# Performance work log

Hardware: AMD Instinct MI355X
Metric: run time of the kernel (lower is better)

Reference implementation:

```python
import jax, jax.numpy as jnp
import numpy as np

VOCAB, N_CLASS, H, E = 50000, 6, 512, 300
B, S = 256, 512


def setup_inputs() -> dict:
    key = jax.random.key(0)
    ks = jax.random.split(key, 10)
    return {
        "seq": jax.random.randint(ks[0], (B, S), 0, VOCAB),
        "classes": jnp.arange(N_CLASS),
        "embed_W": jax.random.normal(ks[1], (VOCAB, E), jnp.float32) * 0.1,
        "embed_class_W": jax.random.normal(ks[2], (N_CLASS, H), jnp.float32) * 0.1,
        "W_ih": jax.random.normal(ks[3], (3 * H, E), jnp.float32) * 0.05,
        "W_hh": jax.random.normal(ks[4], (3 * H, H), jnp.float32) * 0.05,
        "b_ih": jax.random.normal(ks[5], (3 * H,), jnp.float32) * 0.05,
        "b_hh": jax.random.normal(ks[6], (3 * H,), jnp.float32) * 0.05,
        "attend": jax.random.normal(ks[7], (H, H), jnp.float32) * 0.1,
        "W_cls": jax.random.normal(ks[8], (2, H), jnp.float32) * 0.05,
        "b_cls": jax.random.normal(ks[9], (2,), jnp.float32) * 0.05,
    }


def _gru_scan(xs, W_ih, W_hh, b_ih, b_hh):
    # xs: [S, B, E]; torch GRUCell semantics
    h0 = jnp.zeros((xs.shape[1], W_hh.shape[1]), xs.dtype)

    def step(h, x):
        gi = x @ W_ih.T + b_ih            # [B, 3H]
        gh = h @ W_hh.T + b_hh            # [B, 3H]
        i_r, i_z, i_n = jnp.split(gi, 3, axis=-1)
        h_r, h_z, h_n = jnp.split(gh, 3, axis=-1)
        r = jax.nn.sigmoid(i_r + h_r)
        z = jax.nn.sigmoid(i_z + h_z)
        n = jnp.tanh(i_n + r * h_n)
        h_new = (1.0 - z) * n + z * h
        return h_new, h_new

    _, hs = jax.lax.scan(step, h0, xs)
    return hs  # [S, B, H]


def reference(seq, classes, embed_W, embed_class_W, W_ih, W_hh, b_ih, b_hh,
              attend, W_cls, b_cls):
    pad_mask = (seq > 0).astype(embed_W.dtype)          # [B, S]
    seq_emb = jnp.tanh(embed_W[seq])                    # [B, S, E]
    hs = _gru_scan(seq_emb.transpose(1, 0, 2), W_ih, W_hh, b_ih, b_hh)
    seq_repr = hs.transpose(1, 0, 2)                    # [B, S, H]

    class_emb = embed_class_W[classes]                  # [C, H]
    attn = jnp.tanh(class_emb) @ attend                 # [C, H]
    # scores[c,b,s] = tanh(attn)[c] . seq_repr[b,s], masked
    scores = jnp.einsum('ch,bsh->cbs', jnp.tanh(attn), seq_repr)
    scores = scores * pad_mask[None, :, :]
    ctx = jnp.einsum('cbs,bsh->cbh', jnp.tanh(scores), seq_repr)  # [C, B, H]
    logits = jnp.tanh(ctx) @ W_cls.T + b_cls            # [C, B, 2]
    return jax.nn.log_softmax(logits, axis=-1)
```

## Files before the change

### kernel.cpp

```cpp
#include <hip/hip_runtime.h>
#include <cstdint>
#include <cstddef>

#define NB 256
#define NS 512
#define NE 300
#define NH 512

using f32x4 = __attribute__((ext_vector_type(4))) float;
using s16x8 = __attribute__((ext_vector_type(8))) short;

static __device__ __forceinline__ unsigned short f2bf(float f) {
  unsigned u = __float_as_uint(f);
  u += 0x7FFFu + ((u >> 16) & 1u);
  return (unsigned short)(u >> 16);
}
static __device__ __forceinline__ float bf2f(unsigned short h) {
  return __uint_as_float(((unsigned)h) << 16);
}
static __device__ __forceinline__ float fast_tanh(float x) {
  float xc = fminf(fmaxf(x, -9.f), 9.f);
  float e = __expf(2.f * xc);
  return (e - 1.f) / (e + 1.f);
}
static __device__ __forceinline__ float sigm(float x) {
  return 1.f / (1.f + __expf(-x));
}

__global__ void k_zero(unsigned short* __restrict__ h_ex, unsigned* __restrict__ flags) {
  int i = blockIdx.x * 256 + threadIdx.x;
  unsigned long long* p = (unsigned long long*)(h_ex + (size_t)i * 16);
  #pragma unroll
  for (int j = 0; j < 4; ++j)
    __hip_atomic_store(p + j, 0ull, __ATOMIC_RELAXED, __HIP_MEMORY_SCOPE_AGENT);
  if (i < 4096)
    __hip_atomic_store(flags + i, 0u, __ATOMIC_RELAXED, __HIP_MEMORY_SCOPE_AGENT);
}

__global__ __launch_bounds__(256) void k_xemb(const int* __restrict__ seq,
                                              const float* __restrict__ embed_W,
                                              unsigned short* __restrict__ x_pre) {
  const long long total = (long long)NB * NS * 40;
  for (long long t = (long long)blockIdx.x * 256 + threadIdx.x; t < total;
       t += (long long)gridDim.x * 256) {
    int c = (int)(t % 40);
    long long p = t / 40;
    int s = (int)(p % NS);
    int b = (int)(p / NS);
    int g_b = b >> 4, r = b & 15;
    float vals[8];
    if (c < 38) {
      int id = seq[(size_t)b * NS + s];
      const float* ep = embed_W + (size_t)id * NE;
      if (c < 37) {
        f32x4 u0 = *(const f32x4*)(ep + c * 8);
        f32x4 u1 = *(const f32x4*)(ep + c * 8 + 4);
        vals[0]=u0[0];vals[1]=u0[1];vals[2]=u0[2];vals[3]=u0[3];
        vals[4]=u1[0];vals[5]=u1[1];vals[6]=u1[2];vals[7]=u1[3];
      } else {
        #pragma unroll
        for (int jj = 0; jj < 8; ++jj) { int cc = 296 + jj; vals[jj] = (cc < NE) ? ep[cc] : 0.f; }
      }
    } else {
      #pragma unroll
      for (int jj = 0; jj < 8; ++jj) vals[jj] = 0.f;
    }
    s16x8 pv;
    #pragma unroll
    for (int jj = 0; jj < 8; ++jj) pv[jj] = (short)f2bf(fast_tanh(vals[jj]));
    *(s16x8*)(x_pre + (((size_t)g_b * NS + s) * 16 + r) * 320 + c * 8) = pv;
  }
}

__global__ __launch_bounds__(256) void k_amat(const int* __restrict__ classes,
                                              const float* __restrict__ ecw,
                                              const float* __restrict__ attend,
                                              unsigned short* __restrict__ a_bf) {
  __shared__ float tc[6][512];
  const int tid = threadIdx.x, j = blockIdx.x;
  for (int i = tid; i < 6 * 512; i += 256) {
    int c = i >> 9, hp = i & 511;
    tc[c][hp] = fast_tanh(ecw[(size_t)classes[c] * 512 + hp]);
  }
  __syncthreads();
  #pragma unroll
  for (int i = 0; i < 4; ++i) {
    int task = tid + 256 * i;
    int c = task >> 6, hl = task & 63;
    int h = j * 64 + hl;
    float v = 0.f;
    if (c < 6) {
      float acc = 0.f;
      for (int hp = 0; hp < 512; ++hp) acc += tc[c][hp] * attend[(size_t)hp * 512 + h];
      v = fast_tanh(acc);
    }
    a_bf[c * 512 + h] = f2bf(v);
  }
}

__global__ __launch_bounds__(384) void k_gru(
    const int* __restrict__ seq, const float* __restrict__ embed_W,
    const float* __restrict__ W_ih, const float* __restrict__ W_hh,
    const float* __restrict__ b_ih, const float* __restrict__ b_hh,
    unsigned short* __restrict__ h_ex, unsigned* __restrict__ flags,
    unsigned short* __restrict__ seq_repr,
    const unsigned short* __restrict__ x_pre, int xpre)
{
  __shared__ unsigned short x_lds[2][16][328];
  __shared__ unsigned short h_lds[16][520];
  __shared__ float rz_lds[2][16][32];

  const int tid = threadIdx.x;
  const int w = tid >> 6, l = tid & 63, lo = l & 15, hi = l >> 4;
  const int bid = blockIdx.x;
  const int g_b = (bid & 7) * 2 + (bid >> 7);
  const int g_c = (bid >> 3) & 15;

  const int gg = w >> 1;
  const int cb = (w & 1) * 16;
  const int jrow = gg * 512 + g_c * 32 + cb + lo;

  s16x8 whh[16];
  #pragma unroll
  for (int kt = 0; kt < 16; ++kt) {
    const float* p = W_hh + (size_t)jrow * 512 + kt * 32 + hi * 8;
    f32x4 a0 = *(const f32x4*)p;
    f32x4 a1 = *(const f32x4*)(p + 4);
    s16x8 v;
    v[0]=(short)f2bf(a0[0]); v[1]=(short)f2bf(a0[1]); v[2]=(short)f2bf(a0[2]); v[3]=(short)f2bf(a0[3]);
    v[4]=(short)f2bf(a1[0]); v[5]=(short)f2bf(a1[1]); v[6]=(short)f2bf(a1[2]); v[7]=(short)f2bf(a1[3]);
    whh[kt] = v;
  }
  s16x8 wih[10];
  #pragma unroll
  for (int kt = 0; kt < 10; ++kt) {
    s16x8 v;
    #pragma unroll
    for (int jj = 0; jj < 8; ++jj) {
      int k = kt * 32 + hi * 8 + jj;
      float f = (k < NE) ? W_ih[(size_t)jrow * NE + k] : 0.f;
      v[jj] = (short)f2bf(f);
    }
    wih[kt] = v;
  }
  const float bsum = b_ih[jrow] + b_hh[jrow];
  const float bni = b_ih[jrow], bnh = b_hh[jrow];

  float hcar[4] = {0.f, 0.f, 0.f, 0.f};
  const unsigned* flg = flags + g_b * 32;

  const int xt = tid - 64;
  const int xr0 = (xt >= 0) ? (xt / 40) : 0,          xc0 = (xt >= 0) ? (xt % 40) : 0;
  const int xr1 = (xt >= 0) ? ((xt + 320) / 40) : 0,  xc1 = (xt >= 0) ? ((xt + 320) % 40) : 0;

  auto do_gather = [&](int ss) {
    const int buf = ss & 1;
    #pragma unroll
    for (int i = 0; i < 2; ++i) {
      int task = tid + 384 * i;
      if (task < 640) {
        int r = task & 15, grp = task >> 4;
        float vals[8];
        if (grp < 38) {
          int id = seq[(size_t)(g_b * 16 + r) * NS + ss];
          const float* ep = embed_W + (size_t)id * NE;
          if (grp < 37) {
            f32x4 u0 = *(const f32x4*)(ep + grp * 8);
            f32x4 u1 = *(const f32x4*)(ep + grp * 8 + 4);
            vals[0]=u0[0];vals[1]=u0[1];vals[2]=u0[2];vals[3]=u0[3];
            vals[4]=u1[0];vals[5]=u1[1];vals[6]=u1[2];vals[7]=u1[3];
          } else {
            #pragma unroll
            for (int jj = 0; jj < 8; ++jj) { int cc = 296 + jj; vals[jj] = (cc < NE) ? ep[cc] : 0.f; }
          }
        } else {
          #pragma unroll
          for (int jj = 0; jj < 8; ++jj) vals[jj] = 0.f;
        }
        s16x8 pv;
        #pragma unroll
        for (int jj = 0; jj < 8; ++jj) pv[jj] = (short)f2bf(fast_tanh(vals[jj]));
        *(s16x8*)&x_lds[buf][r][grp * 8] = pv;
      }
    }
  };

  if (xpre) {
    if (w >= 1) {
      const unsigned short* src = x_pre + ((size_t)g_b * NS + 0) * (16 * 320);
      s16x8 v0 = *(const s16x8*)(src + xr0 * 320 + xc0 * 8);
      s16x8 v1 = *(const s16x8*)(src + xr1 * 320 + xc1 * 8);
      *(s16x8*)&x_lds[0][xr0][xc0 * 8] = v0;
      *(s16x8*)&x_lds[0][xr1][xc1 * 8] = v1;
    }
  } else {
    do_gather(0);
  }
  __syncthreads();

  #pragma unroll 1
  for (int s = 0; s < NS; ++s) {
    const bool xpf = xpre && (s + 1 < NS) && (w >= 1);
    s16x8 xv0, xv1;
    if (xpf) {
      const unsigned short* src = x_pre + ((size_t)g_b * NS + (s + 1)) * (16 * 320);
      xv0 = *(const s16x8*)(src + xr0 * 320 + xc0 * 8);
      xv1 = *(const s16x8*)(src + xr1 * 320 + xc1 * 8);
    } else if (!xpre && s + 1 < NS) {
      do_gather(s + 1);
    }

    f32x4 ax = {0.f,0.f,0.f,0.f};
    #pragma unroll
    for (int kt = 0; kt < 10; ++kt) {
      s16x8 af = *(const s16x8*)&x_lds[s & 1][lo][kt * 32 + hi * 8];
      ax = __builtin_amdgcn_mfma_f32_16x16x32_bf16(af, wih[kt], ax, 0, 0, 0);
    }

    if (s > 0 && tid < 64) {
      const unsigned* fp = flg + (l & 31);
      int guard = 0;
      for (;;) {
        unsigned f = __hip_atomic_load(fp, __ATOMIC_RELAXED, __HIP_MEMORY_SCOPE_AGENT);
        if (__all(f >= (unsigned)s)) break;
        __builtin_amdgcn_s_sleep(1);
        if (++guard > (1 << 22)) break;
      }
    }
    __syncthreads();

    const unsigned short* hsrc = h_ex + ((size_t)(s & 1) * 16 + g_b) * (16 * 512);
    #pragma unroll
    for (int i = 0; i < 6; ++i) {
      int task = tid + 384 * i;
      if (task < 2048) {
        int r = task >> 7, c4 = task & 127;
        unsigned long long v = __hip_atomic_load(
            (const unsigned long long*)(hsrc + r * 512 + c4 * 4),
            __ATOMIC_RELAXED, __HIP_MEMORY_SCOPE_AGENT);
        *(unsigned long long*)&h_lds[r][c4 * 4] = v;
      }
    }
    __syncthreads();

    if (xpf) {
      *(s16x8*)&x_lds[(s + 1) & 1][xr0][xc0 * 8] = xv0;
      *(s16x8*)&x_lds[(s + 1) & 1][xr1][xc1 * 8] = xv1;
    }

    f32x4 ah0 = {0.f,0.f,0.f,0.f}, ah1 = {0.f,0.f,0.f,0.f};
    #pragma unroll
    for (int kt = 0; kt < 16; kt += 2) {
      s16x8 af0 = *(const s16x8*)&h_lds[lo][kt * 32 + hi * 8];
      s16x8 af1 = *(const s16x8*)&h_lds[lo][(kt + 1) * 32 + hi * 8];
      ah0 = __builtin_amdgcn_mfma_f32_16x16x32_bf16(af0, whh[kt], ah0, 0, 0, 0);
      ah1 = __builtin_amdgcn_mfma_f32_16x16x32_bf16(af1, whh[kt + 1], ah1, 0, 0, 0);
    }
    f32x4 ah = ah0 + ah1;

    if (w < 4) {
      #pragma unroll
      for (int j = 0; j < 4; ++j) {
        int row = hi * 4 + j;
        rz_lds[gg][row][cb + lo] = ax[j] + ah[j] + bsum;
      }
    }
    __syncthreads();

    if (w >= 4) {
      unsigned short* hdst = h_ex + ((size_t)((s + 1) & 1) * 16 + g_b) * (16 * 512);
      const int cpr = cb + lo;
      const int col = g_c * 32 + cpr;
      unsigned words[4];
      #pragma unroll
      for (int j = 0; j < 4; ++j) {
        int row = hi * 4 + j;
        float rr = sigm(rz_lds[0][row][cpr]);
        float zz = sigm(rz_lds[1][row][cpr]);
        float nn = fast_tanh(ax[j] + bni + rr * (ah[j] + bnh));
        float hn = (1.f - zz) * nn + zz * hcar[j];
        hcar[j] = hn;
        unsigned myb = (unsigned)f2bf(hn);
        unsigned other = __shfl_xor(myb, 1);
        words[j] = myb | (other << 16);
      }
      if ((lo & 1) == 0) {
        #pragma unroll
        for (int j = 0; j < 4; ++j)
          __hip_atomic_store((unsigned*)(hdst + (hi * 4 + j) * 512 + col), words[j],
                             __ATOMIC_RELAXED, __HIP_MEMORY_SCOPE_AGENT);
      }
      asm volatile("s_waitcnt vmcnt(0)" ::: "memory");
      if (l == 0)
        __hip_atomic_store((unsigned*)(flags + g_b * 32 + g_c * 2 + (w & 1)),
                           (unsigned)(s + 1),
                           __ATOMIC_RELAXED, __HIP_MEMORY_SCOPE_AGENT);
      if ((lo & 1) == 0) {
        #pragma unroll
        for (int j = 0; j < 4; ++j)
          *(unsigned*)(seq_repr + ((size_t)(g_b * 16 + hi * 4 + j) * NS + s) * NH + col) = words[j];
      }
    }
  }
}

__global__ __launch_bounds__(256) void k_attn(const int* __restrict__ seq,
                                              const unsigned short* __restrict__ seq_repr,
                                              const unsigned short* __restrict__ a_bf,
                                              const float* __restrict__ W_cls,
                                              const float* __restrict__ b_cls,
                                              float* __restrict__ out)
{
  __shared__ unsigned short V[32][520];
  __shared__ float P[32][8];
  __shared__ float red[4][12];
  const int tid = threadIdx.x, b = blockIdx.x;
  const int w = tid >> 6, l = tid & 63, lo = l & 15, hi = l >> 4;

  s16x8 afr[16];
  #pragma unroll
  for (int kt = 0; kt < 16; ++kt)
    afr[kt] = *(const s16x8*)(a_bf + (size_t)lo * 512 + kt * 32 + hi * 8);

  float ctx0[6] = {0,0,0,0,0,0}, ctx1[6] = {0,0,0,0,0,0};
  const unsigned short* vbase = seq_repr + (size_t)b * NS * NH;

  for (int sc = 0; sc < 16; ++sc) {
    #pragma unroll 4
    for (int i = 0; i < 8; ++i) {
      int task = tid + 256 * i;
      int sl = task >> 6, grp = task & 63;
      s16x8 v = *(const s16x8*)(vbase + (size_t)(sc * 32 + sl) * NH + grp * 8);
      *(s16x8*)&V[sl][grp * 8] = v;
    }
    __syncthreads();
    if (w < 2) {
      f32x4 acc = {0.f,0.f,0.f,0.f};
      int sl0 = w * 16;
      #pragma unroll
      for (int kt = 0; kt < 16; ++kt) {
        s16x8 af = *(const s16x8*)&V[sl0 + lo][kt * 32 + hi * 8];
        acc = __builtin_amdgcn_mfma_f32_16x16x32_bf16(af, afr[kt], acc, 0, 0, 0);
      }
      if (lo < 8) {
        #pragma unroll
        for (int j = 0; j < 4; ++j) {
          int sl = sl0 + hi * 4 + j;
          float p = 0.f;
          if (lo < 6) {
            int s = sc * 32 + sl;
            p = (seq[(size_t)b * NS + s] > 0) ? fast_tanh(acc[j]) : 0.f;
          }
          P[sl][lo] = p;
        }
      }
    }
    __syncthreads();
    #pragma unroll 2
    for (int sl = 0; sl < 32; ++sl) {
      unsigned v2 = *(const unsigned*)&V[sl][tid * 2];
      float v0 = bf2f((unsigned short)(v2 & 0xFFFFu));
      float v1 = bf2f((unsigned short)(v2 >> 16));
      #pragma unroll
      for (int c = 0; c < 6; ++c) {
        float p = P[sl][c];
        ctx0[c] += p * v0; ctx1[c] += p * v1;
      }
    }
    __syncthreads();
  }

  float pl[12];
  #pragma unroll
  for (int c = 0; c < 6; ++c) {
    float t0 = fast_tanh(ctx0[c]), t1 = fast_tanh(ctx1[c]);
    pl[c * 2 + 0] = t0 * W_cls[tid * 2] + t1 * W_cls[tid * 2 + 1];
    pl[c * 2 + 1] = t0 * W_cls[512 + tid * 2] + t1 * W_cls[512 + tid * 2 + 1];
  }
  #pragma unroll
  for (int i = 0; i < 12; ++i) {
    float v = pl[i];
    for (int off = 32; off > 0; off >>= 1) v += __shfl_down(v, off);
    if (l == 0) red[w][i] = v;
  }
  __syncthreads();
  if (tid < 6) {
    int c = tid;
    float l0 = red[0][c*2] + red[1][c*2] + red[2][c*2] + red[3][c*2] + b_cls[0];
    float l1 = red[0][c*2+1] + red[1][c*2+1] + red[2][c*2+1] + red[3][c*2+1] + b_cls[1];
    float m = fmaxf(l0, l1);
    float lse = m + logf(__expf(l0 - m) + __expf(l1 - m));
    out[c * 512 + b * 2 + 0] = l0 - lse;
    out[c * 512 + b * 2 + 1] = l1 - lse;
  }
}

extern "C" void kernel_launch(void* const* d_in, const int* in_sizes, int n_in,
                              void* d_out, int out_size, void* d_ws, size_t ws_size,
                              hipStream_t stream) {
  const int*   seq      = (const int*)d_in[0];
  const int*   classes  = (const int*)d_in[1];
  const float* embed_W  = (const float*)d_in[2];
  const float* ecw      = (const float*)d_in[3];
  const float* W_ih     = (const float*)d_in[4];
  const float* W_hh     = (const float*)d_in[5];
  const float* b_ih     = (const float*)d_in[6];
  const float* b_hh     = (const float*)d_in[7];
  const float* attend   = (const float*)d_in[8];
  const float* W_cls    = (const float*)d_in[9];
  const float* b_cls    = (const float*)d_in[10];
  float* out = (float*)d_out;

  char* ws = (char*)d_ws;
  const size_t OFF_HEX  = 134217728;
  const size_t OFF_FLG  = OFF_HEX + 524288;
  const size_t OFF_ABF  = OFF_FLG + 16384;
  const size_t OFF_XPRE = OFF_ABF + 16384;
  const size_t XPRE_BYTES = (size_t)16 * NS * 16 * 320 * 2;
  unsigned short* seq_repr = (unsigned short*)ws;
  unsigned short* h_ex     = (unsigned short*)(ws + OFF_HEX);
  unsigned*       flags    = (unsigned*)(ws + OFF_FLG);
  unsigned short* a_bf     = (unsigned short*)(ws + OFF_ABF);
  unsigned short* x_pre    = (unsigned short*)(ws + OFF_XPRE);
  const int xpre = (ws_size >= OFF_XPRE + XPRE_BYTES) ? 1 : 0;

  hipLaunchKernelGGL(k_zero, dim3(64), dim3(256), 0, stream, h_ex, flags);
  hipLaunchKernelGGL(k_amat, dim3(8), dim3(256), 0, stream, classes, ecw, attend, a_bf);
  if (xpre)
    hipLaunchKernelGGL(k_xemb, dim3(2048), dim3(256), 0, stream, seq, embed_W, x_pre);
  hipLaunchKernelGGL(k_gru, dim3(256), dim3(384), 0, stream,
                     seq, embed_W, W_ih, W_hh, b_ih, b_hh, h_ex, flags, seq_repr,
                     x_pre, xpre);
  hipLaunchKernelGGL(k_attn, dim3(256), dim3(256), 0, stream,
                     seq, seq_repr, a_bf, W_cls, b_cls, out);
}
```

Measured before the change: 2.244 ms.

## Replace flag-based step barrier with step-tagged hidden-state words

Each bf16 hidden value is now stored in a 32-bit word with the step number in its upper half. Consumers load the whole hidden tile and re-poll only the words whose tag does not match yet, so the separate flag array, the vmcnt drain and the flag store are gone. This removes a store-then-flag round trip and a pre-read barrier from the recurrent critical path. In exchange, the hidden exchange buffer doubles in size, every thread spins on global memory, and the spin-loop guard is much lower than before.

```diff
diff --git a/kernel.cpp b/kernel.cpp
--- a/kernel.cpp
+++ b/kernel.cpp
@@ -27,14 +27,12 @@
   return 1.f / (1.f + __expf(-x));
 }
 
-__global__ void k_zero(unsigned short* __restrict__ h_ex, unsigned* __restrict__ flags) {
+__global__ void k_zero(unsigned* __restrict__ h_w) {
   int i = blockIdx.x * 256 + threadIdx.x;
-  unsigned long long* p = (unsigned long long*)(h_ex + (size_t)i * 16);
-  #pragma unroll
-  for (int j = 0; j < 4; ++j)
+  unsigned long long* p = (unsigned long long*)(h_w + (size_t)i * 16);
+  #pragma unroll
+  for (int j = 0; j < 8; ++j)
     __hip_atomic_store(p + j, 0ull, __ATOMIC_RELAXED, __HIP_MEMORY_SCOPE_AGENT);
-  if (i < 4096)
-    __hip_atomic_store(flags + i, 0u, __ATOMIC_RELAXED, __HIP_MEMORY_SCOPE_AGENT);
 }
 
 __global__ __launch_bounds__(256) void k_xemb(const int* __restrict__ seq,
@@ -102,8 +100,7 @@
     const int* __restrict__ seq, const float* __restrict__ embed_W,
     const float* __restrict__ W_ih, const float* __restrict__ W_hh,
     const float* __restrict__ b_ih, const float* __restrict__ b_hh,
-    unsigned short* __restrict__ h_ex, unsigned* __restrict__ flags,
-    unsigned short* __restrict__ seq_repr,
+    unsigned* __restrict__ h_w, unsigned short* __restrict__ seq_repr,
     const unsigned short* __restrict__ x_pre, int xpre)
 {
   __shared__ unsigned short x_lds[2][16][328];
@@ -147,7 +144,6 @@
   const float bni = b_ih[jrow], bnh = b_hh[jrow];
 
   float hcar[4] = {0.f, 0.f, 0.f, 0.f};
-  const unsigned* flg = flags + g_b * 32;
 
   const int xt = tid - 64;
   const int xr0 = (xt >= 0) ? (xt / 40) : 0,          xc0 = (xt >= 0) ? (xt % 40) : 0;
@@ -217,28 +213,45 @@
       ax = __builtin_amdgcn_mfma_f32_16x16x32_bf16(af, wih[kt], ax, 0, 0, 0);
     }
 
-    if (s > 0 && tid < 64) {
-      const unsigned* fp = flg + (l & 31);
+    {
+      const unsigned long long* hw =
+          (const unsigned long long*)(h_w + ((size_t)(s & 1) * 16 + g_b) * (16 * 512));
+      const unsigned tagp = (unsigned)s & 0xFFFFu;
+      unsigned long long hv[11];
+      unsigned need = 0;
+      #pragma unroll
+      for (int i = 0; i < 11; ++i) {
+        int task = tid + 384 * i;
+        if (task < 4096) {
+          hv[i] = __hip_atomic_load(hw + task, __ATOMIC_RELAXED, __HIP_MEMORY_SCOPE_AGENT);
+          need |= 1u << i;
+        }
+      }
       int guard = 0;
       for (;;) {
-        unsigned f = __hip_atomic_load(fp, __ATOMIC_RELAXED, __HIP_MEMORY_SCOPE_AGENT);
-        if (__all(f >= (unsigned)s)) break;
-        __builtin_amdgcn_s_sleep(1);
-        if (++guard > (1 << 22)) break;
-      }
-    }
-    __syncthreads();
-
-    const unsigned short* hsrc = h_ex + ((size_t)(s & 1) * 16 + g_b) * (16 * 512);
-    #pragma unroll
-    for (int i = 0; i < 6; ++i) {
-      int task = tid + 384 * i;
-      if (task < 2048) {
-        int r = task >> 7, c4 = task & 127;
-        unsigned long long v = __hip_atomic_load(
-            (const unsigned long long*)(hsrc + r * 512 + c4 * 4),
-            __ATOMIC_RELAXED, __HIP_MEMORY_SCOPE_AGENT);
-        *(unsigned long long*)&h_lds[r][c4 * 4] = v;
+        unsigned bad = 0;
+        #pragma unroll
+        for (int i = 0; i < 11; ++i) if (need & (1u << i)) {
+          unsigned t0 = (unsigned)(hv[i] >> 16) & 0xFFFFu;
+          unsigned t1 = (unsigned)(hv[i] >> 48);
+          if (t0 != tagp || t1 != tagp) bad |= 1u << i;
+        }
+        if (!bad) break;
+        #pragma unroll
+        for (int i = 0; i < 11; ++i) if (bad & (1u << i))
+          hv[i] = __hip_atomic_load(hw + tid + 384 * i, __ATOMIC_RELAXED, __HIP_MEMORY_SCOPE_AGENT);
+        need = bad;
+        if (++guard > (1 << 13)) break;
+      }
+      #pragma unroll
+      for (int i = 0; i < 11; ++i) {
+        int task = tid + 384 * i;
+        if (task < 4096) {
+          int r = task >> 8, c2 = task & 255;
+          unsigned packed = ((unsigned)(hv[i] & 0xFFFFu)) |
+                            (((unsigned)(hv[i] >> 32) & 0xFFFFu) << 16);
+          *(unsigned*)&h_lds[r][c2 * 2] = packed;
+        }
       }
     }
     __syncthreads();
@@ -268,10 +281,11 @@
     __syncthreads();
 
     if (w >= 4) {
-      unsigned short* hdst = h_ex + ((size_t)((s + 1) & 1) * 16 + g_b) * (16 * 512);
+      unsigned* hdst = h_w + ((size_t)((s + 1) & 1) * 16 + g_b) * (16 * 512);
       const int cpr = cb + lo;
       const int col = g_c * 32 + cpr;
-      unsigned words[4];
+      const unsigned tagn = ((unsigned)(s + 1) & 0xFFFFu) << 16;
+      unsigned mybs[4];
       #pragma unroll
       for (int j = 0; j < 4; ++j) {
         int row = hi * 4 + j;
@@ -281,24 +295,17 @@
         float hn = (1.f - zz) * nn + zz * hcar[j];
         hcar[j] = hn;
         unsigned myb = (unsigned)f2bf(hn);
-        unsigned other = __shfl_xor(myb, 1);
-        words[j] = myb | (other << 16);
-      }
-      if ((lo & 1) == 0) {
-        #pragma unroll
-        for (int j = 0; j < 4; ++j)
-          __hip_atomic_store((unsigned*)(hdst + (hi * 4 + j) * 512 + col), words[j],
-                             __ATOMIC_RELAXED, __HIP_MEMORY_SCOPE_AGENT);
-      }
-      asm volatile("s_waitcnt vmcnt(0)" ::: "memory");
-      if (l == 0)
-        __hip_atomic_store((unsigned*)(flags + g_b * 32 + g_c * 2 + (w & 1)),
-                           (unsigned)(s + 1),
+        mybs[j] = myb;
+        __hip_atomic_store(hdst + row * 512 + col, tagn | myb,
                            __ATOMIC_RELAXED, __HIP_MEMORY_SCOPE_AGENT);
-      if ((lo & 1) == 0) {
-        #pragma unroll
-        for (int j = 0; j < 4; ++j)
-          *(unsigned*)(seq_repr + ((size_t)(g_b * 16 + hi * 4 + j) * NS + s) * NH + col) = words[j];
+      }
+      #pragma unroll
+      for (int j = 0; j < 4; ++j) {
+        unsigned other = __shfl_xor(mybs[j], 1);
+        if ((lo & 1) == 0) {
+          unsigned word = mybs[j] | (other << 16);
+          *(unsigned*)(seq_repr + ((size_t)(g_b * 16 + hi * 4 + j) * NS + s) * NH + col) = word;
+        }
       }
     }
   }
@@ -412,24 +419,22 @@
   float* out = (float*)d_out;
 
   char* ws = (char*)d_ws;
-  const size_t OFF_HEX  = 134217728;
-  const size_t OFF_FLG  = OFF_HEX + 524288;
-  const size_t OFF_ABF  = OFF_FLG + 16384;
+  const size_t OFF_HW   = 134217728;
+  const size_t OFF_ABF  = OFF_HW + 1048576;
   const size_t OFF_XPRE = OFF_ABF + 16384;
   const size_t XPRE_BYTES = (size_t)16 * NS * 16 * 320 * 2;
   unsigned short* seq_repr = (unsigned short*)ws;
-  unsigned short* h_ex     = (unsigned short*)(ws + OFF_HEX);
-  unsigned*       flags    = (unsigned*)(ws + OFF_FLG);
+  unsigned*       h_w      = (unsigned*)(ws + OFF_HW);
   unsigned short* a_bf     = (unsigned short*)(ws + OFF_ABF);
   unsigned short* x_pre    = (unsigned short*)(ws + OFF_XPRE);
   const int xpre = (ws_size >= OFF_XPRE + XPRE_BYTES) ? 1 : 0;
 
-  hipLaunchKernelGGL(k_zero, dim3(64), dim3(256), 0, stream, h_ex, flags);
+  hipLaunchKernelGGL(k_zero, dim3(64), dim3(256), 0, stream, h_w);
   hipLaunchKernelGGL(k_amat, dim3(8), dim3(256), 0, stream, classes, ecw, attend, a_bf);
   if (xpre)
     hipLaunchKernelGGL(k_xemb, dim3(2048), dim3(256), 0, stream, seq, embed_W, x_pre);
   hipLaunchKernelGGL(k_gru, dim3(256), dim3(384), 0, stream,
-                     seq, embed_W, W_ih, W_hh, b_ih, b_hh, h_ex, flags, seq_repr,
+                     seq, embed_W, W_ih, W_hh, b_ih, b_hh, h_w, seq_repr,
                      x_pre, xpre);
   hipLaunchKernelGGL(k_attn, dim3(256), dim3(256), 0, stream,
                      seq, seq_repr, a_bf, W_cls, b_cls, out);
```

After: 2.726 ms. 21.5% more time.

## Add dedicated polling wavefront to GRU recurrence to separate flag spin from compute

Applied to the files above, without the earlier changes.

Adds a seventh wavefront per block of the persistent GRU kernel whose only job is to spin on the cross-block step flags, without sleeping, and help load the shared hidden state into LDS. The six compute wavefronts no longer poll; they issue the input MFMAs and meet the poller at the barrier. The aim is to cut per-step synchronisation latency by polling tightly and freeing the compute waves. The cost is an extra wave per block, busy-spinning memory traffic, and a matched barrier count between the two paths that must stay aligned.

```diff
diff --git a/kernel.cpp b/kernel.cpp
--- a/kernel.cpp
+++ b/kernel.cpp
@@ -98,7 +98,7 @@
   }
 }
 
-__global__ __launch_bounds__(384) void k_gru(
+__global__ __launch_bounds__(448) void k_gru(
     const int* __restrict__ seq, const float* __restrict__ embed_W,
     const float* __restrict__ W_ih, const float* __restrict__ W_hh,
     const float* __restrict__ b_ih, const float* __restrict__ b_hh,
@@ -112,52 +112,57 @@
 
   const int tid = threadIdx.x;
   const int w = tid >> 6, l = tid & 63, lo = l & 15, hi = l >> 4;
+  const bool cw = (w < 6);
   const int bid = blockIdx.x;
   const int g_b = (bid & 7) * 2 + (bid >> 7);
   const int g_c = (bid >> 3) & 15;
 
-  const int gg = w >> 1;
+  const int gg = (w < 6) ? (w >> 1) : 0;
   const int cb = (w & 1) * 16;
-  const int jrow = gg * 512 + g_c * 32 + cb + lo;
+  const int jrow = cw ? (gg * 512 + g_c * 32 + cb + lo) : 0;
 
   s16x8 whh[16];
-  #pragma unroll
-  for (int kt = 0; kt < 16; ++kt) {
-    const float* p = W_hh + (size_t)jrow * 512 + kt * 32 + hi * 8;
-    f32x4 a0 = *(const f32x4*)p;
-    f32x4 a1 = *(const f32x4*)(p + 4);
-    s16x8 v;
-    v[0]=(short)f2bf(a0[0]); v[1]=(short)f2bf(a0[1]); v[2]=(short)f2bf(a0[2]); v[3]=(short)f2bf(a0[3]);
-    v[4]=(short)f2bf(a1[0]); v[5]=(short)f2bf(a1[1]); v[6]=(short)f2bf(a1[2]); v[7]=(short)f2bf(a1[3]);
-    whh[kt] = v;
-  }
   s16x8 wih[10];
-  #pragma unroll
-  for (int kt = 0; kt < 10; ++kt) {
-    s16x8 v;
+  float bsum = 0.f, bni = 0.f, bnh = 0.f;
+  if (cw) {
     #pragma unroll
-    for (int jj = 0; jj < 8; ++jj) {
-      int k = kt * 32 + hi * 8 + jj;
-      float f = (k < NE) ? W_ih[(size_t)jrow * NE + k] : 0.f;
-      v[jj] = (short)f2bf(f);
-    }
-    wih[kt] = v;
-  }
-  const float bsum = b_ih[jrow] + b_hh[jrow];
-  const float bni = b_ih[jrow], bnh = b_hh[jrow];
+    for (int kt = 0; kt < 16; ++kt) {
+      const float* p = W_hh + (size_t)jrow * 512 + kt * 32 + hi * 8;
+      f32x4 a0 = *(const f32x4*)p;
+      f32x4 a1 = *(const f32x4*)(p + 4);
+      s16x8 v;
+      v[0]=(short)f2bf(a0[0]); v[1]=(short)f2bf(a0[1]); v[2]=(short)f2bf(a0[2]); v[3]=(short)f2bf(a0[3]);
+      v[4]=(short)f2bf(a1[0]); v[5]=(short)f2bf(a1[1]); v[6]=(short)f2bf(a1[2]); v[7]=(short)f2bf(a1[3]);
+      whh[kt] = v;
+    }
+    #pragma unroll
+    for (int kt = 0; kt < 10; ++kt) {
+      s16x8 v;
+      #pragma unroll
+      for (int jj = 0; jj < 8; ++jj) {
+        int k = kt * 32 + hi * 8 + jj;
+        float f = (k < NE) ? W_ih[(size_t)jrow * NE + k] : 0.f;
+        v[jj] = (short)f2bf(f);
+      }
+      wih[kt] = v;
+    }
+    bsum = b_ih[jrow] + b_hh[jrow];
+    bni = b_ih[jrow]; bnh = b_hh[jrow];
+  }
 
   float hcar[4] = {0.f, 0.f, 0.f, 0.f};
   const unsigned* flg = flags + g_b * 32;
 
   const int xt = tid - 64;
-  const int xr0 = (xt >= 0) ? (xt / 40) : 0,          xc0 = (xt >= 0) ? (xt % 40) : 0;
-  const int xr1 = (xt >= 0) ? ((xt + 320) / 40) : 0,  xc1 = (xt >= 0) ? ((xt + 320) % 40) : 0;
+  const bool xw = (w >= 1 && w < 6);
+  const int xr0 = xw ? (xt / 40) : 0,          xc0 = xw ? (xt % 40) : 0;
+  const int xr1 = xw ? ((xt + 320) / 40) : 0,  xc1 = xw ? ((xt + 320) % 40) : 0;
 
   auto do_gather = [&](int ss) {
     const int buf = ss & 1;
     #pragma unroll
     for (int i = 0; i < 2; ++i) {
-      int task = tid + 384 * i;
+      int task = tid + 448 * i;
       if (task < 640) {
         int r = task & 15, grp = task >> 4;
         float vals[8];
@@ -186,7 +191,7 @@
   };
 
   if (xpre) {
-    if (w >= 1) {
+    if (xw) {
       const unsigned short* src = x_pre + ((size_t)g_b * NS + 0) * (16 * 320);
       s16x8 v0 = *(const s16x8*)(src + xr0 * 320 + xc0 * 8);
       s16x8 v1 = *(const s16x8*)(src + xr1 * 320 + xc1 * 8);
@@ -200,108 +205,128 @@
 
   #pragma unroll 1
   for (int s = 0; s < NS; ++s) {
-    const bool xpf = xpre && (s + 1 < NS) && (w >= 1);
-    s16x8 xv0, xv1;
-    if (xpf) {
-      const unsigned short* src = x_pre + ((size_t)g_b * NS + (s + 1)) * (16 * 320);
-      xv0 = *(const s16x8*)(src + xr0 * 320 + xc0 * 8);
-      xv1 = *(const s16x8*)(src + xr1 * 320 + xc1 * 8);
-    } else if (!xpre && s + 1 < NS) {
-      do_gather(s + 1);
-    }
-
-    f32x4 ax = {0.f,0.f,0.f,0.f};
-    #pragma unroll
-    for (int kt = 0; kt < 10; ++kt) {
-      s16x8 af = *(const s16x8*)&x_lds[s & 1][lo][kt * 32 + hi * 8];
-      ax = __builtin_amdgcn_mfma_f32_16x16x32_bf16(af, wih[kt], ax, 0, 0, 0);
-    }
-
-    if (s > 0 && tid < 64) {
-      const unsigned* fp = flg + (l & 31);
-      int guard = 0;
-      for (;;) {
-        unsigned f = __hip_atomic_load(fp, __ATOMIC_RELAXED, __HIP_MEMORY_SCOPE_AGENT);
-        if (__all(f >= (unsigned)s)) break;
-        __builtin_amdgcn_s_sleep(1);
-        if (++guard > (1 << 22)) break;
-      }
-    }
-    __syncthreads();
-
-    const unsigned short* hsrc = h_ex + ((size_t)(s & 1) * 16 + g_b) * (16 * 512);
-    #pragma unroll
-    for (int i = 0; i < 6; ++i) {
-      int task = tid + 384 * i;
-      if (task < 2048) {
-        int r = task >> 7, c4 = task & 127;
-        unsigned long long v = __hip_atomic_load(
-            (const unsigned long long*)(hsrc + r * 512 + c4 * 4),
-            __ATOMIC_RELAXED, __HIP_MEMORY_SCOPE_AGENT);
-        *(unsigned long long*)&h_lds[r][c4 * 4] = v;
-      }
-    }
-    __syncthreads();
-
-    if (xpf) {
-      *(s16x8*)&x_lds[(s + 1) & 1][xr0][xc0 * 8] = xv0;
-      *(s16x8*)&x_lds[(s + 1) & 1][xr1][xc1 * 8] = xv1;
-    }
-
-    f32x4 ah0 = {0.f,0.f,0.f,0.f}, ah1 = {0.f,0.f,0.f,0.f};
-    #pragma unroll
-    for (int kt = 0; kt < 16; kt += 2) {
-      s16x8 af0 = *(const s16x8*)&h_lds[lo][kt * 32 + hi * 8];
-      s16x8 af1 = *(const s16x8*)&h_lds[lo][(kt + 1) * 32 + hi * 8];
-      ah0 = __builtin_amdgcn_mfma_f32_16x16x32_bf16(af0, whh[kt], ah0, 0, 0, 0);
-      ah1 = __builtin_amdgcn_mfma_f32_16x16x32_bf16(af1, whh[kt + 1], ah1, 0, 0, 0);
-    }
-    f32x4 ah = ah0 + ah1;
-
-    if (w < 4) {
-      #pragma unroll
-      for (int j = 0; j < 4; ++j) {
-        int row = hi * 4 + j;
-        rz_lds[gg][row][cb + lo] = ax[j] + ah[j] + bsum;
-      }
-    }
-    __syncthreads();
-
-    if (w >= 4) {
-      unsigned short* hdst = h_ex + ((size_t)((s + 1) & 1) * 16 + g_b) * (16 * 512);
-      const int cpr = cb + lo;
-      const int col = g_c * 32 + cpr;
-      unsigned words[4];
-      #pragma unroll
-      for (int j = 0; j < 4; ++j) {
-        int row = hi * 4 + j;
-        float rr = sigm(rz_lds[0][row][cpr]);
-        float zz = sigm(rz_lds[1][row][cpr]);
-        float nn = fast_tanh(ax[j] + bni + rr * (ah[j] + bnh));
-        float hn = (1.f - zz) * nn + zz * hcar[j];
-        hcar[j] = hn;
-        unsigned myb = (unsigned)f2bf(hn);
-        unsigned other = __shfl_xor(myb, 1);
-        words[j] = myb | (other << 16);
-      }
-      if ((lo & 1) == 0) {
+    if (!cw) {
+      if (s > 0) {
+        const unsigned* fp = flg + (l & 31);
+        int guard = 0;
+        for (;;) {
+          unsigned f = __hip_atomic_load(fp, __ATOMIC_RELAXED, __HIP_MEMORY_SCOPE_AGENT);
+          if (__all(f >= (unsigned)s)) break;
+          if (++guard > (1 << 22)) break;
+        }
+      }
+    } else {
+      const bool xpf = xpre && (s + 1 < NS) && xw;
+      s16x8 xv0, xv1;
+      if (xpf) {
+        const unsigned short* src = x_pre + ((size_t)g_b * NS + (s + 1)) * (16 * 320);
+        xv0 = *(const s16x8*)(src + xr0 * 320 + xc0 * 8);
+        xv1 = *(const s16x8*)(src + xr1 * 320 + xc1 * 8);
+      } else if (!xpre && s + 1 < NS) {
+        do_gather(s + 1);
+      }
+      f32x4 ax_ = {0.f,0.f,0.f,0.f};
+      #pragma unroll
+      for (int kt = 0; kt < 10; ++kt) {
+        s16x8 af = *(const s16x8*)&x_lds[s & 1][lo][kt * 32 + hi * 8];
+        ax_ = __builtin_amdgcn_mfma_f32_16x16x32_bf16(af, wih[kt], ax_, 0, 0, 0);
+      }
+      __syncthreads();
+
+      const unsigned short* hsrc = h_ex + ((size_t)(s & 1) * 16 + g_b) * (16 * 512);
+      #pragma unroll
+      for (int i = 0; i < 5; ++i) {
+        int task = tid + 448 * i;
+        if (task < 2048) {
+          int r = task >> 7, c4 = task & 127;
+          unsigned long long v = __hip_atomic_load(
+              (const unsigned long long*)(hsrc + r * 512 + c4 * 4),
+              __ATOMIC_RELAXED, __HIP_MEMORY_SCOPE_AGENT);
+          *(unsigned long long*)&h_lds[r][c4 * 4] = v;
+        }
+      }
+      __syncthreads();
+
+      if (xpf) {
+        *(s16x8*)&x_lds[(s + 1) & 1][xr0][xc0 * 8] = xv0;
+        *(s16x8*)&x_lds[(s + 1) & 1][xr1][xc1 * 8] = xv1;
+      }
+
+      f32x4 ah0 = {0.f,0.f,0.f,0.f}, ah1 = {0.f,0.f,0.f,0.f};
+      #pragma unroll
+      for (int kt = 0; kt < 16; kt += 2) {
+        s16x8 af0 = *(const s16x8*)&h_lds[lo][kt * 32 + hi * 8];
+        s16x8 af1 = *(const s16x8*)&h_lds[lo][(kt + 1) * 32 + hi * 8];
+        ah0 = __builtin_amdgcn_mfma_f32_16x16x32_bf16(af0, whh[kt], ah0, 0, 0, 0);
+        ah1 = __builtin_amdgcn_mfma_f32_16x16x32_bf16(af1, whh[kt + 1], ah1, 0, 0, 0);
+      }
+      f32x4 ah = ah0 + ah1;
+
+      if (w < 4) {
         #pragma unroll
-        for (int j = 0; j < 4; ++j)
-          __hip_atomic_store((unsigned*)(hdst + (hi * 4 + j) * 512 + col), words[j],
+        for (int j = 0; j < 4; ++j) {
+          int row = hi * 4 + j;
+          rz_lds[gg][row][cb + lo] = ax_[j] + ah[j] + bsum;
+        }
+      }
+      __syncthreads();
+
+      if (w >= 4) {
+        unsigned short* hdst = h_ex + ((size_t)((s + 1) & 1) * 16 + g_b) * (16 * 512);
+        const int cpr = cb + lo;
+        const int col = g_c * 32 + cpr;
+        unsigned words[4];
+        #pragma unroll
+        for (int j = 0; j < 4; ++j) {
+          int row = hi * 4 + j;
+          float rr = sigm(rz_lds[0][row][cpr]);
+          float zz = sigm(rz_lds[1][row][cpr]);
+          float nn = fast_tanh(ax_[j] + bni + rr * (ah[j] + bnh));
+          float hn = (1.f - zz) * nn + zz * hcar[j];
+          hcar[j] = hn;
+          unsigned myb = (unsigned)f2bf(hn);
+          unsigned other = __shfl_xor(myb, 1);
+          words[j] = myb | (other << 16);
+        }
+        if ((lo & 1) == 0) {
+          #pragma unroll
+          for (int j = 0; j < 4; ++j)
+            __hip_atomic_store((unsigned*)(hdst + (hi * 4 + j) * 512 + col), words[j],
+                               __ATOMIC_RELAXED, __HIP_MEMORY_SCOPE_AGENT);
+        }
+        asm volatile("s_waitcnt vmcnt(0)" ::: "memory");
+        if (l == 0)
+          __hip_atomic_store((unsigned*)(flags + g_b * 32 + g_c * 2 + (w & 1)),
+                             (unsigned)(s + 1),
                              __ATOMIC_RELAXED, __HIP_MEMORY_SCOPE_AGENT);
-      }
-      asm volatile("s_waitcnt vmcnt(0)" ::: "memory");
-      if (l == 0)
-        __hip_atomic_store((unsigned*)(flags + g_b * 32 + g_c * 2 + (w & 1)),
-                           (unsigned)(s + 1),
-                           __ATOMIC_RELAXED, __HIP_MEMORY_SCOPE_AGENT);
-      if ((lo & 1) == 0) {
-        #pragma unroll
-        for (int j = 0; j < 4; ++j)
-          *(unsigned*)(seq_repr + ((size_t)(g_b * 16 + hi * 4 + j) * NS + s) * NH + col) = words[j];
-      }
-    }
-  }
+        if ((lo & 1) == 0) {
+          #pragma unroll
+          for (int j = 0; j < 4; ++j)
+            *(unsigned*)(seq_repr + ((size_t)(g_b * 16 + hi * 4 + j) * NS + s) * NH + col) = words[j];
+        }
+      }
+      continue;
+    }
+
+    __syncthreads();
+    {
+      const unsigned short* hsrc = h_ex + ((size_t)(s & 1) * 16 + g_b) * (16 * 512);
+      #pragma unroll
+      for (int i = 0; i < 5; ++i) {
+        int task = tid + 448 * i;
+        if (task < 2048) {
+          int r = task >> 7, c4 = task & 127;
+          unsigned long long v = __hip_atomic_load(
+              (const unsigned long long*)(hsrc + r * 512 + c4 * 4),
+              __ATOMIC_RELAXED, __HIP_MEMORY_SCOPE_AGENT);
+          *(unsigned long long*)&h_lds[r][c4 * 4] = v;
+        }
+      }
+    }
+    __syncthreads();
+    __syncthreads();
+  }
+
 }
 
 __global__ __launch_bounds__(256) void k_attn(const int* __restrict__ seq,
@@ -428,7 +453,7 @@
   hipLaunchKernelGGL(k_amat, dim3(8), dim3(256), 0, stream, classes, ecw, attend, a_bf);
   if (xpre)
     hipLaunchKernelGGL(k_xemb, dim3(2048), dim3(256), 0, stream, seq, embed_W, x_pre);
-  hipLaunchKernelGGL(k_gru, dim3(256), dim3(384), 0, stream,
+  hipLaunchKernelGGL(k_gru, dim3(256), dim3(448), 0, stream,
                      seq, embed_W, W_ih, W_hh, b_ih, b_hh, h_ex, flags, seq_repr,
                      x_pre, xpre);
   hipLaunchKernelGGL(k_attn, dim3(256), dim3(256), 0, stream,
```

Result: faster. 2.152 ms (-4.1%).

## Replace per-step block barriers with per-slice flag polling and LDS done flags

Applied to the files above, without the earlier changes.

Instead of one wave polling all 32 producer flags and then two block-wide barriers before loading the whole hidden state, each wave now polls only the flags for its assigned 32-column slices. It loads those slices into a double-buffered h_lds and signals per-slice readiness through LDS done flags. The MFMA loop waits on each slice flag, so hidden-state matmul work can start as soon as individual slices arrive, which removes barrier latency from the serial recurrence. This adds spin loops on LDS, removes s_sleep from the global poll, and lowers the guard counts, so a slow producer could exit the wait early and read stale data. LDS use also grows.

```diff
diff --git a/kernel.cpp b/kernel.cpp
--- a/kernel.cpp
+++ b/kernel.cpp
@@ -107,8 +107,9 @@
     const unsigned short* __restrict__ x_pre, int xpre)
 {
   __shared__ unsigned short x_lds[2][16][328];
-  __shared__ unsigned short h_lds[16][520];
+  __shared__ unsigned short h_lds[2][16][520];
   __shared__ float rz_lds[2][16][32];
+  __shared__ unsigned done[2][16];
 
   const int tid = threadIdx.x;
   const int w = tid >> 6, l = tid & 63, lo = l & 15, hi = l >> 4;
@@ -150,8 +151,9 @@
   const unsigned* flg = flags + g_b * 32;
 
   const int xt = tid - 64;
-  const int xr0 = (xt >= 0) ? (xt / 40) : 0,          xc0 = (xt >= 0) ? (xt % 40) : 0;
-  const int xr1 = (xt >= 0) ? ((xt + 320) / 40) : 0,  xc1 = (xt >= 0) ? ((xt + 320) % 40) : 0;
+  const bool xw = (w >= 1);
+  const int xr0 = xw ? (xt / 40) : 0,          xc0 = xw ? (xt % 40) : 0;
+  const int xr1 = xw ? ((xt + 320) / 40) : 0,  xc1 = xw ? ((xt + 320) % 40) : 0;
 
   auto do_gather = [&](int ss) {
     const int buf = ss & 1;
@@ -185,8 +187,9 @@
     }
   };
 
+  if (tid < 32) ((volatile unsigned*)&done[0][0])[tid] = 0u;
   if (xpre) {
-    if (w >= 1) {
+    if (xw) {
       const unsigned short* src = x_pre + ((size_t)g_b * NS + 0) * (16 * 320);
       s16x8 v0 = *(const s16x8*)(src + xr0 * 320 + xc0 * 8);
       s16x8 v1 = *(const s16x8*)(src + xr1 * 320 + xc1 * 8);
@@ -200,7 +203,17 @@
 
   #pragma unroll 1
   for (int s = 0; s < NS; ++s) {
-    const bool xpf = xpre && (s + 1 < NS) && (w >= 1);
+    const int par = s & 1;
+    if (l == 0) {
+      #pragma unroll
+      for (int c = 0; c < 3; ++c) {
+        int p = w + 6 * c;
+        if (p < 16)
+          __hip_atomic_store(&done[par ^ 1][p], 0u, __ATOMIC_RELAXED, __HIP_MEMORY_SCOPE_WORKGROUP);
+      }
+    }
+
+    const bool xpf = xpre && (s + 1 < NS) && xw;
     s16x8 xv0, xv1;
     if (xpf) {
       const unsigned short* src = x_pre + ((size_t)g_b * NS + (s + 1)) * (16 * 320);
@@ -209,66 +222,83 @@
     } else if (!xpre && s + 1 < NS) {
       do_gather(s + 1);
     }
-
-    f32x4 ax = {0.f,0.f,0.f,0.f};
+    f32x4 ax_ = {0.f,0.f,0.f,0.f};
     #pragma unroll
     for (int kt = 0; kt < 10; ++kt) {
-      s16x8 af = *(const s16x8*)&x_lds[s & 1][lo][kt * 32 + hi * 8];
-      ax = __builtin_amdgcn_mfma_f32_16x16x32_bf16(af, wih[kt], ax, 0, 0, 0);
-    }
-
-    if (s > 0 && tid < 64) {
-      const unsigned* fp = flg + (l & 31);
-      int guard = 0;
-      for (;;) {
-        unsigned f = __hip_atomic_load(fp, __ATOMIC_RELAXED, __HIP_MEMORY_SCOPE_AGENT);
-        if (__all(f >= (unsigned)s)) break;
-        __builtin_amdgcn_s_sleep(1);
-        if (++guard > (1 << 22)) break;
-      }
-    }
-    __syncthreads();
-
-    const unsigned short* hsrc = h_ex + ((size_t)(s & 1) * 16 + g_b) * (16 * 512);
-    #pragma unroll
-    for (int i = 0; i < 6; ++i) {
-      int task = tid + 384 * i;
-      if (task < 2048) {
-        int r = task >> 7, c4 = task & 127;
-        unsigned long long v = __hip_atomic_load(
-            (const unsigned long long*)(hsrc + r * 512 + c4 * 4),
+      s16x8 af = *(const s16x8*)&x_lds[par][lo][kt * 32 + hi * 8];
+      ax_ = __builtin_amdgcn_mfma_f32_16x16x32_bf16(af, wih[kt], ax_, 0, 0, 0);
+    }
+
+    const unsigned short* hsrc = h_ex + ((size_t)par * 16 + g_b) * (16 * 512);
+    #pragma unroll
+    for (int c = 0; c < 3; ++c) {
+      int p = w + 6 * c;
+      if (p < 16) {
+        if (s > 0) {
+          const unsigned* fp = flg + p * 2 + (l & 1);
+          int guard = 0;
+          for (;;) {
+            unsigned f = __hip_atomic_load(fp, __ATOMIC_RELAXED, __HIP_MEMORY_SCOPE_AGENT);
+            if (__all(f >= (unsigned)s)) break;
+            if (++guard > (1 << 14)) break;
+          }
+        }
+        int j0 = l, j1 = l + 64;
+        unsigned long long v0 = __hip_atomic_load(
+            (const unsigned long long*)(hsrc + (j0 >> 3) * 512 + p * 32 + (j0 & 7) * 4),
             __ATOMIC_RELAXED, __HIP_MEMORY_SCOPE_AGENT);
-        *(unsigned long long*)&h_lds[r][c4 * 4] = v;
-      }
-    }
-    __syncthreads();
+        unsigned long long v1 = __hip_atomic_load(
+            (const unsigned long long*)(hsrc + (j1 >> 3) * 512 + p * 32 + (j1 & 7) * 4),
+            __ATOMIC_RELAXED, __HIP_MEMORY_SCOPE_AGENT);
+        *(unsigned long long*)&h_lds[par][j0 >> 3][p * 32 + (j0 & 7) * 4] = v0;
+        *(unsigned long long*)&h_lds[par][j1 >> 3][p * 32 + (j1 & 7) * 4] = v1;
+        if (l == 0)
+          __hip_atomic_store(&done[par][p], 1u, __ATOMIC_RELEASE, __HIP_MEMORY_SCOPE_WORKGROUP);
+      }
+    }
+
+    f32x4 ah0 = {0.f,0.f,0.f,0.f}, ah1 = {0.f,0.f,0.f,0.f};
+    #pragma unroll
+    for (int p = 0; p < 16; p += 2) {
+      {
+        int g2 = 0;
+        for (;;) {
+          unsigned d = __hip_atomic_load(&done[par][p], __ATOMIC_ACQUIRE, __HIP_MEMORY_SCOPE_WORKGROUP);
+          if (d) break;
+          if (++g2 > (1 << 16)) break;
+        }
+        s16x8 af = *(const s16x8*)&h_lds[par][lo][p * 32 + hi * 8];
+        ah0 = __builtin_amdgcn_mfma_f32_16x16x32_bf16(af, whh[p], ah0, 0, 0, 0);
+      }
+      {
+        int g2 = 0;
+        for (;;) {
+          unsigned d = __hip_atomic_load(&done[par][p + 1], __ATOMIC_ACQUIRE, __HIP_MEMORY_SCOPE_WORKGROUP);
+          if (d) break;
+          if (++g2 > (1 << 16)) break;
+        }
+        s16x8 af = *(const s16x8*)&h_lds[par][lo][(p + 1) * 32 + hi * 8];
+        ah1 = __builtin_amdgcn_mfma_f32_16x16x32_bf16(af, whh[p + 1], ah1, 0, 0, 0);
+      }
+    }
+    f32x4 ah = ah0 + ah1;
 
     if (xpf) {
-      *(s16x8*)&x_lds[(s + 1) & 1][xr0][xc0 * 8] = xv0;
-      *(s16x8*)&x_lds[(s + 1) & 1][xr1][xc1 * 8] = xv1;
-    }
-
-    f32x4 ah0 = {0.f,0.f,0.f,0.f}, ah1 = {0.f,0.f,0.f,0.f};
-    #pragma unroll
-    for (int kt = 0; kt < 16; kt += 2) {
-      s16x8 af0 = *(const s16x8*)&h_lds[lo][kt * 32 + hi * 8];
-      s16x8 af1 = *(const s16x8*)&h_lds[lo][(kt + 1) * 32 + hi * 8];
-      ah0 = __builtin_amdgcn_mfma_f32_16x16x32_bf16(af0, whh[kt], ah0, 0, 0, 0);
-      ah1 = __builtin_amdgcn_mfma_f32_16x16x32_bf16(af1, whh[kt + 1], ah1, 0, 0, 0);
-    }
-    f32x4 ah = ah0 + ah1;
+      *(s16x8*)&x_lds[par ^ 1][xr0][xc0 * 8] = xv0;
+      *(s16x8*)&x_lds[par ^ 1][xr1][xc1 * 8] = xv1;
+    }
 
     if (w < 4) {
       #pragma unroll
       for (int j = 0; j < 4; ++j) {
         int row = hi * 4 + j;
-        rz_lds[gg][row][cb + lo] = ax[j] + ah[j] + bsum;
+        rz_lds[gg][row][cb + lo] = ax_[j] + ah[j] + bsum;
       }
     }
     __syncthreads();
 
     if (w >= 4) {
-      unsigned short* hdst = h_ex + ((size_t)((s + 1) & 1) * 16 + g_b) * (16 * 512);
+      unsigned short* hdst = h_ex + ((size_t)(par ^ 1) * 16 + g_b) * (16 * 512);
       const int cpr = cb + lo;
       const int col = g_c * 32 + cpr;
       unsigned words[4];
@@ -277,17 +307,14 @@
         int row = hi * 4 + j;
         float rr = sigm(rz_lds[0][row][cpr]);
         float zz = sigm(rz_lds[1][row][cpr]);
-        float nn = fast_tanh(ax[j] + bni + rr * (ah[j] + bnh));
+        float nn = fast_tanh(ax_[j] + bni + rr * (ah[j] + bnh));
         float hn = (1.f - zz) * nn + zz * hcar[j];
         hcar[j] = hn;
         unsigned myb = (unsigned)f2bf(hn);
         unsigned other = __shfl_xor(myb, 1);
         words[j] = myb | (other << 16);
-      }
-      if ((lo & 1) == 0) {
-        #pragma unroll
-        for (int j = 0; j < 4; ++j)
-          __hip_atomic_store((unsigned*)(hdst + (hi * 4 + j) * 512 + col), words[j],
+        if ((lo & 1) == 0)
+          __hip_atomic_store((unsigned*)(hdst + row * 512 + col), words[j],
                              __ATOMIC_RELAXED, __HIP_MEMORY_SCOPE_AGENT);
       }
       asm volatile("s_waitcnt vmcnt(0)" ::: "memory");
```

Result: slower. 4.463 ms (+98.9%).
